# Kernel optimization log

Measured on AMD Instinct MI355X. Metric: run time of the kernel, lower is better.

The kernel has to match this reference:

```python
import jax, jax.numpy as jnp
import numpy as np

NUM_EXPERTS = 64
TOP_K = 8
LOAD_EMA_DECAY = 0.999
BIAS_TEMPERATURE = 1.0
NOISE_STD = 0.01


def setup_inputs() -> dict:
    key = jax.random.key(0)
    k1, k2, k3, k4 = jax.random.split(key, 4)
    hidden_states = jax.random.normal(k1, (4, 4096, 2048), dtype=jnp.float32)
    router_w = jax.random.normal(k2, (NUM_EXPERTS, 2048), dtype=jnp.float32) * 0.02
    expert_loads = jax.random.uniform(k3, (NUM_EXPERTS,), dtype=jnp.float32)
    bias_strength = jnp.ones((1,), dtype=jnp.float32)
    noise = jax.random.normal(k4, (4 * 4096, NUM_EXPERTS), dtype=jnp.float32)
    return {
        "hidden_states": hidden_states,
        "router_w": router_w,
        "expert_loads": expert_loads,
        "bias_strength": bias_strength,
        "noise": noise,
    }


def reference(hidden_states, router_w, expert_loads, bias_strength, noise):
    # Training-mode forward with total_routed > 0 (adaptive bias active),
    # balance_loss_weight = 0 (aux_loss is None in the original).
    E = NUM_EXPERTS
    x = hidden_states.reshape(-1, hidden_states.shape[-1])  # [N, d]
    n_tokens = x.shape[0]

    # Router linear (no bias) + training noise
    logits = jnp.einsum("nd,ed->ne", x, router_w) + noise * NOISE_STD  # [N, E]

    # Adaptive load-based bias (core of aux-loss-free routing)
    q = expert_loads / jnp.clip(expert_loads.sum(), 1e-8)  # normalized loads
    t = 1.0 / E  # expected uniform load
    # F.kl_div(log q, t, reduction='sum') = sum_e t*(log t - log q_e)
    kl = jnp.sum(t * (jnp.log(t) - jnp.log(jnp.clip(q, 1e-8))))
    adaptive_strength = jax.nn.sigmoid(kl * 10.0)
    new_bias_strength = 0.9 * bias_strength[0] + 0.1 * adaptive_strength
    bias = jnp.tanh((q - t) * E) * BIAS_TEMPERATURE * new_bias_strength  # [E]
    logits = logits - bias[None, :]

    # Top-k selection + softmax gating over selected logits
    expert_weights, expert_indices = jax.lax.top_k(logits, TOP_K)  # [N, K]
    expert_weights = jax.nn.softmax(expert_weights, axis=-1)

    # EMA load-statistics update (scatter-add of gate weights per expert)
    batch_loads = jax.ops.segment_sum(
        expert_weights.reshape(-1), expert_indices.reshape(-1), num_segments=E
    ) / n_tokens
    new_expert_loads = LOAD_EMA_DECAY * expert_loads + (1.0 - LOAD_EMA_DECAY) * batch_loads

    return expert_indices, expert_weights, new_expert_loads, new_bias_strength
```

## Files before the change

### kernel.cpp

```cpp
#include <hip/hip_runtime.h>
#include <math.h>

#define NT 16384
#define DIM 2048
#define NE 64
#define TK 8

typedef _Float16 f16_t;
typedef _Float16 half8 __attribute__((ext_vector_type(8)));
typedef float floatx16 __attribute__((ext_vector_type(16)));

__global__ __launch_bounds__(256) void prep_kernel(const float* __restrict__ w,
                                                   const float* __restrict__ expert_loads,
                                                   const float* __restrict__ bias_strength,
                                                   float* __restrict__ ws_bias,
                                                   float* __restrict__ ws_batch,
                                                   f16_t* __restrict__ whi,
                                                   f16_t* __restrict__ wlo,
                                                   float* __restrict__ out_bias_strength) {
    if (blockIdx.x == 64) {
        int e = threadIdx.x;
        if (e < 64) {
            float load = expert_loads[e];
            float s = load;
            #pragma unroll
            for (int off = 32; off >= 1; off >>= 1) s += __shfl_xor(s, off, 64);
            s = fmaxf(s, 1e-8f);
            float q = load / s;
            const float t = 1.0f / 64.0f;
            float kl = t * (logf(t) - logf(fmaxf(q, 1e-8f)));
            #pragma unroll
            for (int off = 32; off >= 1; off >>= 1) kl += __shfl_xor(kl, off, 64);
            float as = 1.0f / (1.0f + expf(-10.0f * kl));
            float nbs = 0.9f * bias_strength[0] + 0.1f * as;
            ws_bias[e] = tanhf((q - t) * 64.0f) * nbs;
            ws_batch[e] = 0.0f;
            if (e == 0) out_bias_strength[0] = nbs;
        }
        return;
    }
    int idx = blockIdx.x * 256 + threadIdx.x;
    int lane = idx & 63;
    int tile = (idx >> 6) & 1;
    int c    = idx >> 7;
    int n = tile * 32 + (lane & 31);
    int k = c * 16 + (lane >> 5) * 8;
    const float* src = w + (size_t)n * DIM + k;
    float4 a = *(const float4*)src;
    float4 b = *(const float4*)(src + 4);
    float v[8] = {a.x, a.y, a.z, a.w, b.x, b.y, b.z, b.w};
    half8 h, l;
    #pragma unroll
    for (int j = 0; j < 8; ++j) {
        f16_t hh = (f16_t)v[j];
        h[j] = hh;
        l[j] = (f16_t)(v[j] - (float)hh);
    }
    *(half8*)(whi + (size_t)idx * 8) = h;
    *(half8*)(wlo + (size_t)idx * 8) = l;
}

__global__ __launch_bounds__(512, 4) void router_main(const float* __restrict__ x,
                                                      const f16_t* __restrict__ whi,
                                                      const f16_t* __restrict__ wlo,
                                                      const float* __restrict__ noise,
                                                      const float* __restrict__ ws_bias,
                                                      float* __restrict__ ws_batch,
                                                      float* __restrict__ out) {
    __shared__ float smem[17408];
    __shared__ float bias_sh[64];
    __shared__ float loads_sh[64];

    const int tid = threadIdx.x;
    const int wv  = tid >> 6;
    const int L   = tid & 63;
    const int r   = L & 31;
    const int kh  = L >> 5;
    const int sw  = r & 7;
    const int token0 = blockIdx.x * 32;

    if (tid < 64) { bias_sh[tid] = ws_bias[tid]; loads_sh[tid] = 0.0f; }

    float4 nz = *(const float4*)(noise + (size_t)token0 * NE + tid * 4);

    const half8* whi8 = (const half8*)whi;
    const half8* wlo8 = (const half8*)wlo;

    floatx16 acc0, acc1;
    #pragma unroll
    for (int i = 0; i < 16; ++i) { acc0[i] = 0.0f; acc1[i] = 0.0f; }

    auto STAGE = [&](int S) {
        const int b_ = S & 1;
        #pragma unroll
        for (int q = 0; q < 4; ++q) {
            const float* gsrc = x + (size_t)(token0 + q * 8 + (L >> 3)) * DIM
                                  + wv * 256 + S * 32 + (((L & 7) ^ ((L >> 3) & 7)) << 2);
            float* ldst = (float*)(smem + wv * 2048 + b_ * 1024 + q * 256);
            __builtin_amdgcn_global_load_lds(
                (const __attribute__((address_space(1))) unsigned int*)gsrc,
                (__attribute__((address_space(3))) unsigned int*)ldst,
                16, 0, 0);
        }
    };

    STAGE(0);

    #pragma unroll
    for (int s = 0; s < 8; ++s) {
        half8 bf[8];
        {
            const int c0 = wv * 16 + s * 2;
            const int i0 = (c0 * 2) * 64 + L;
            const int i1 = ((c0 + 1) * 2) * 64 + L;
            bf[0] = whi8[i0];      bf[1] = whi8[i0 + 64];
            bf[2] = wlo8[i0];      bf[3] = wlo8[i0 + 64];
            bf[4] = whi8[i1];      bf[5] = whi8[i1 + 64];
            bf[6] = wlo8[i1];      bf[7] = wlo8[i1 + 64];
        }
        if (s < 7) {
            STAGE(s + 1);
            asm volatile("s_waitcnt vmcnt(12)" ::: "memory");
        } else {
            asm volatile("s_waitcnt vmcnt(8)" ::: "memory");
        }

        const float* wb = smem + wv * 2048 + (s & 1) * 1024;
        #pragma unroll
        for (int cc = 0; cc < 2; ++cc) {
            const int u  = kh * 2 + cc * 4;
            const int pu = (u ^ sw);
            float4 f0 = *(const float4*)(wb + r * 32 + (pu << 2));
            float4 f1 = *(const float4*)(wb + r * 32 + ((pu ^ 1) << 2));
            float v[8] = {f0.x, f0.y, f0.z, f0.w, f1.x, f1.y, f1.z, f1.w};
            half8 ah, al;
            #pragma unroll
            for (int j = 0; j < 8; ++j) {
                f16_t hh = (f16_t)v[j];
                ah[j] = hh;
                al[j] = (f16_t)(v[j] - (float)hh);
            }
            acc0 = __builtin_amdgcn_mfma_f32_32x32x16_f16(ah, bf[cc * 4 + 0], acc0, 0, 0, 0);
            acc1 = __builtin_amdgcn_mfma_f32_32x32x16_f16(ah, bf[cc * 4 + 1], acc1, 0, 0, 0);
            acc0 = __builtin_amdgcn_mfma_f32_32x32x16_f16(al, bf[cc * 4 + 0], acc0, 0, 0, 0);
            acc1 = __builtin_amdgcn_mfma_f32_32x32x16_f16(al, bf[cc * 4 + 1], acc1, 0, 0, 0);
            acc0 = __builtin_amdgcn_mfma_f32_32x32x16_f16(ah, bf[cc * 4 + 2], acc0, 0, 0, 0);
            acc1 = __builtin_amdgcn_mfma_f32_32x32x16_f16(ah, bf[cc * 4 + 3], acc1, 0, 0, 0);
        }
    }

    __syncthreads();

    #pragma unroll
    for (int reg = 0; reg < 16; ++reg) {
        int row = (reg & 3) + 8 * (reg >> 2) + 4 * kh;
        smem[wv * 2176 + row * 68 + r]      = acc0[reg];
        smem[wv * 2176 + row * 68 + 32 + r] = acc1[reg];
    }
    __syncthreads();

    float nzv[4] = {nz.x, nz.y, nz.z, nz.w};
    #pragma unroll
    for (int j = 0; j < 4; ++j) {
        int o = tid * 4 + j;
        int t = o >> 6, e = o & 63;
        float sum = 0.0f;
        #pragma unroll
        for (int q = 0; q < 8; ++q) sum += smem[q * 2176 + t * 68 + e];
        sum += nzv[j] * 0.01f - bias_sh[e];
        smem[t * 68 + e] = sum;
    }
    __syncthreads();

    if (tid < 32) {
        int t = tid;
        float tv[TK]; int ti_[TK];
        #pragma unroll
        for (int j = 0; j < TK; ++j) { tv[j] = -INFINITY; ti_[j] = 0; }
        for (int e = 0; e < NE; ++e) {
            float v = smem[t * 68 + e]; int id = e;
            #pragma unroll
            for (int j = 0; j < TK; ++j) {
                bool gt = v > tv[j];
                float nv = gt ? v : tv[j];
                int   ni = gt ? id : ti_[j];
                float ov = gt ? tv[j] : v;
                int   oi = gt ? ti_[j] : id;
                tv[j] = nv; ti_[j] = ni; v = ov; id = oi;
            }
        }
        float m = tv[0], ssum = 0.0f, wvv[TK];
        #pragma unroll
        for (int j = 0; j < TK; ++j) { wvv[j] = expf(tv[j] - m); ssum += wvv[j]; }
        float inv = 1.0f / ssum;
        size_t gt_ = (size_t)(token0 + t);
        #pragma unroll
        for (int j = 0; j < TK; ++j) {
            float wgt = wvv[j] * inv;
            out[gt_ * TK + j] = (float)ti_[j];
            out[(size_t)NT * TK + gt_ * TK + j] = wgt;
            atomicAdd(&loads_sh[ti_[j]], wgt);
        }
    }
    __syncthreads();
    if (tid < 64) atomicAdd(&ws_batch[tid], loads_sh[tid]);
}

__global__ __launch_bounds__(64) void finalize_kernel(const float* __restrict__ expert_loads,
                                                      const float* __restrict__ ws_batch,
                                                      float* __restrict__ out_loads) {
    int e = threadIdx.x;
    out_loads[e] = 0.999f * expert_loads[e] + 0.001f * (ws_batch[e] / (float)NT);
}

extern "C" void kernel_launch(void* const* d_in, const int* in_sizes, int n_in,
                              void* d_out, int out_size, void* d_ws, size_t ws_size,
                              hipStream_t stream) {
    const float* x     = (const float*)d_in[0];
    const float* rw    = (const float*)d_in[1];
    const float* loads = (const float*)d_in[2];
    const float* bs    = (const float*)d_in[3];
    const float* noise = (const float*)d_in[4];
    float* out = (float*)d_out;
    float* ws  = (float*)d_ws;
    float* ws_bias  = ws;
    float* ws_batch = ws + 64;
    f16_t* whi = (f16_t*)(ws + 128);
    f16_t* wlo = whi + (size_t)16384 * 8;

    prep_kernel<<<65, 256, 0, stream>>>(rw, loads, bs, ws_bias, ws_batch, whi, wlo,
                                        out + (size_t)NT * TK * 2 + NE);
    router_main<<<NT / 32, 512, 0, stream>>>(x, whi, wlo, noise, ws_bias, ws_batch, out);
    finalize_kernel<<<1, 64, 0, stream>>>(loads, ws_batch, out + (size_t)NT * TK * 2);
}
```

Baseline: 216.4 us.

## Parallelize top-k across four lanes per token and fuse finalize via last-block counter

Top-k selection now uses four lanes per token, each scanning 16 experts, then merges the partial top-8 lists with shuffle-based bitonic merges instead of one thread scanning all 64 experts. The separate finalize kernel is removed: a global atomic counter detects the last block, which computes the EMA load update in place. This shortens the serial tail of each block and drops one kernel launch, at the cost of extra shuffles and a global atomic with a memory fence per block.

```diff
diff --git a/kernel.cpp b/kernel.cpp
--- a/kernel.cpp
+++ b/kernel.cpp
@@ -15,6 +15,7 @@
                                                    const float* __restrict__ bias_strength,
                                                    float* __restrict__ ws_bias,
                                                    float* __restrict__ ws_batch,
+                                                   unsigned int* __restrict__ ws_counter,
                                                    f16_t* __restrict__ whi,
                                                    f16_t* __restrict__ wlo,
                                                    float* __restrict__ out_bias_strength) {
@@ -35,7 +36,7 @@
             float nbs = 0.9f * bias_strength[0] + 0.1f * as;
             ws_bias[e] = tanhf((q - t) * 64.0f) * nbs;
             ws_batch[e] = 0.0f;
-            if (e == 0) out_bias_strength[0] = nbs;
+            if (e == 0) { out_bias_strength[0] = nbs; ws_counter[0] = 0u; }
         }
         return;
     }
@@ -66,10 +67,13 @@
                                                       const float* __restrict__ noise,
                                                       const float* __restrict__ ws_bias,
                                                       float* __restrict__ ws_batch,
+                                                      unsigned int* __restrict__ ws_counter,
+                                                      const float* __restrict__ expert_loads,
                                                       float* __restrict__ out) {
     __shared__ float smem[17408];
     __shared__ float bias_sh[64];
     __shared__ float loads_sh[64];
+    __shared__ int last_flag;
 
     const int tid = threadIdx.x;
     const int wv  = tid >> 6;
@@ -172,45 +176,100 @@
     }
     __syncthreads();
 
-    if (tid < 32) {
-        int t = tid;
-        float tv[TK]; int ti_[TK];
-        #pragma unroll
-        for (int j = 0; j < TK; ++j) { tv[j] = -INFINITY; ti_[j] = 0; }
-        for (int e = 0; e < NE; ++e) {
-            float v = smem[t * 68 + e]; int id = e;
-            #pragma unroll
-            for (int j = 0; j < TK; ++j) {
-                bool gt = v > tv[j];
-                float nv = gt ? v : tv[j];
-                int   ni = gt ? id : ti_[j];
-                float ov = gt ? tv[j] : v;
-                int   oi = gt ? ti_[j] : id;
-                tv[j] = nv; ti_[j] = ni; v = ov; id = oi;
-            }
-        }
-        float m = tv[0], ssum = 0.0f, wvv[TK];
-        #pragma unroll
-        for (int j = 0; j < TK; ++j) { wvv[j] = expf(tv[j] - m); ssum += wvv[j]; }
-        float inv = 1.0f / ssum;
-        size_t gt_ = (size_t)(token0 + t);
-        #pragma unroll
-        for (int j = 0; j < TK; ++j) {
-            float wgt = wvv[j] * inv;
-            out[gt_ * TK + j] = (float)ti_[j];
-            out[(size_t)NT * TK + gt_ * TK + j] = wgt;
-            atomicAdd(&loads_sh[ti_[j]], wgt);
-        }
-    }
-    __syncthreads();
-    if (tid < 64) atomicAdd(&ws_batch[tid], loads_sh[tid]);
-}
-
-__global__ __launch_bounds__(64) void finalize_kernel(const float* __restrict__ expert_loads,
-                                                      const float* __restrict__ ws_batch,
-                                                      float* __restrict__ out_loads) {
-    int e = threadIdx.x;
-    out_loads[e] = 0.999f * expert_loads[e] + 0.001f * (ws_batch[e] / (float)NT);
+    if (tid < 128) {
+        const int t = tid >> 2;
+        const int m = tid & 3;
+        float av[8]; int ai[8];
+        #pragma unroll
+        for (int j = 0; j < TK; ++j) { av[j] = -INFINITY; ai[j] = 0x7FFFFFFF; }
+        const float* lg = smem + t * 68 + m * 16;
+        float4 q0 = *(const float4*)(lg);
+        float4 q1 = *(const float4*)(lg + 4);
+        float4 q2 = *(const float4*)(lg + 8);
+        float4 q3 = *(const float4*)(lg + 12);
+        float cand[16] = {q0.x, q0.y, q0.z, q0.w, q1.x, q1.y, q1.z, q1.w,
+                          q2.x, q2.y, q2.z, q2.w, q3.x, q3.y, q3.z, q3.w};
+        #pragma unroll
+        for (int e0 = 0; e0 < 16; ++e0) {
+            float v = cand[e0]; int id = m * 16 + e0;
+            #pragma unroll
+            for (int j = 0; j < TK; ++j) {
+                bool gt = v > av[j];
+                float nv = gt ? v : av[j];
+                int   ni = gt ? id : ai[j];
+                float ov = gt ? av[j] : v;
+                int   oi = gt ? ai[j] : id;
+                av[j] = nv; ai[j] = ni; v = ov; id = oi;
+            }
+        }
+        #pragma unroll
+        for (int lvl = 0; lvl < 2; ++lvl) {
+            const int d = 1 << lvl;
+            float pv[8]; int pi[8];
+            #pragma unroll
+            for (int j = 0; j < TK; ++j) {
+                pv[j] = __shfl_xor(av[j], d, 64);
+                pi[j] = __shfl_xor(ai[j], d, 64);
+            }
+            const bool iamA = ((m & d) == 0);
+            float Av[8], Bv[8]; int Ai[8], Bi[8];
+            #pragma unroll
+            for (int j = 0; j < TK; ++j) {
+                Av[j] = iamA ? av[j] : pv[j];  Ai[j] = iamA ? ai[j] : pi[j];
+                Bv[j] = iamA ? pv[j] : av[j];  Bi[j] = iamA ? pi[j] : ai[j];
+            }
+            #pragma unroll
+            for (int j = 0; j < TK; ++j) {
+                float bv = Bv[7 - j]; int bi = Bi[7 - j];
+                bool w = (Av[j] > bv) || (Av[j] == bv && Ai[j] < bi);
+                av[j] = w ? Av[j] : bv;
+                ai[j] = w ? Ai[j] : bi;
+            }
+            #pragma unroll
+            for (int dd = 4; dd >= 1; dd >>= 1) {
+                #pragma unroll
+                for (int j = 0; j < TK; ++j) {
+                    if ((j & dd) == 0) {
+                        int k2 = j + dd;
+                        bool w = (av[j] > av[k2]) || (av[j] == av[k2] && ai[j] < ai[k2]);
+                        float lv = w ? av[j] : av[k2], hv = w ? av[k2] : av[j];
+                        int   li = w ? ai[j] : ai[k2], hi_ = w ? ai[k2] : ai[j];
+                        av[j] = lv; ai[j] = li; av[k2] = hv; ai[k2] = hi_;
+                    }
+                }
+            }
+        }
+        if (m == 0) {
+            float mx = av[0], ssum = 0.0f, wvv[TK];
+            #pragma unroll
+            for (int j = 0; j < TK; ++j) { wvv[j] = expf(av[j] - mx); ssum += wvv[j]; }
+            float inv = 1.0f / ssum;
+            size_t gt_ = (size_t)(token0 + t);
+            #pragma unroll
+            for (int j = 0; j < TK; ++j) {
+                float wgt = wvv[j] * inv;
+                out[gt_ * TK + j] = (float)ai[j];
+                out[(size_t)NT * TK + gt_ * TK + j] = wgt;
+                atomicAdd(&loads_sh[ai[j]], wgt);
+            }
+        }
+    }
+    __syncthreads();
+
+    if (tid < 64) {
+        float old = atomicAdd(&ws_batch[tid], loads_sh[tid]);
+        asm volatile("" :: "v"(old));
+    }
+    if (tid == 0) {
+        asm volatile("s_waitcnt vmcnt(0)" ::: "memory");
+        unsigned int prev = atomicAdd(ws_counter, 1u);
+        last_flag = (prev == (unsigned int)(NT / 32 - 1)) ? 1 : 0;
+    }
+    __syncthreads();
+    if (last_flag && tid < 64) {
+        float bl = atomicAdd(&ws_batch[tid], 0.0f);
+        out[(size_t)NT * TK * 2 + tid] = 0.999f * expert_loads[tid] + 0.001f * (bl / (float)NT);
+    }
 }
 
 extern "C" void kernel_launch(void* const* d_in, const int* in_sizes, int n_in,
@@ -225,11 +284,12 @@
     float* ws  = (float*)d_ws;
     float* ws_bias  = ws;
     float* ws_batch = ws + 64;
-    f16_t* whi = (f16_t*)(ws + 128);
+    unsigned int* ws_counter = (unsigned int*)(ws + 128);
+    f16_t* whi = (f16_t*)(ws + 160);
     f16_t* wlo = whi + (size_t)16384 * 8;
 
-    prep_kernel<<<65, 256, 0, stream>>>(rw, loads, bs, ws_bias, ws_batch, whi, wlo,
+    prep_kernel<<<65, 256, 0, stream>>>(rw, loads, bs, ws_bias, ws_batch, ws_counter, whi, wlo,
                                         out + (size_t)NT * TK * 2 + NE);
-    router_main<<<NT / 32, 512, 0, stream>>>(x, whi, wlo, noise, ws_bias, ws_batch, out);
-    finalize_kernel<<<1, 64, 0, stream>>>(loads, ws_batch, out + (size_t)NT * TK * 2);
+    router_main<<<NT / 32, 512, 0, stream>>>(x, whi, wlo, noise, ws_bias, ws_batch, ws_counter,
+                                             loads, out);
 }
```

Result: no change. 213.0 us (-1.6%).
